# Performance work log

Measured on AMD Instinct MI355X. Metric: run time of the kernel, lower is better.

## Reference

```python
import jax, jax.numpy as jnp
import numpy as np

NU, NI, DIN, DOUT, NS, E = 100000, 100000, 128, 128, 5, 500000


def setup_inputs() -> dict:
    key = jax.random.key(0)
    ks = jax.random.split(key, 9)
    scale = 1.0 / np.sqrt(DIN)
    return {
        "user_inputs": jax.random.normal(ks[0], (NU, DIN), jnp.float32),
        "item_inputs": jax.random.normal(ks[1], (NI, DIN), jnp.float32),
        "weight": jax.random.normal(ks[2], (DIN, DOUT, NS), jnp.float32) * scale,
        "u_rows": jax.random.randint(ks[3], (NS, E), 0, NU),
        "u_cols": jax.random.randint(ks[4], (NS, E), 0, NI),
        "u_vals": jax.random.uniform(ks[5], (NS, E), jnp.float32),
        "i_rows": jax.random.randint(ks[6], (NS, E), 0, NI),
        "i_cols": jax.random.randint(ks[7], (NS, E), 0, NU),
        "i_vals": jax.random.uniform(ks[8], (NS, E), jnp.float32),
    }


def _spmm(rows, cols, vals, dense, n_rows):
    # COO sparse [n_rows, n_cols] @ dense [n_cols, d] -> [n_rows, d]
    msgs = vals[:, None] * dense[cols]  # [E, d]
    return jax.ops.segment_sum(msgs, rows, num_segments=n_rows)


def reference(user_inputs, item_inputs, weight, u_rows, u_cols, u_vals, i_rows, i_cols, i_vals):
    n_users = user_inputs.shape[0]
    n_items = item_inputs.shape[0]
    num_support = weight.shape[-1]
    w = jnp.zeros(weight.shape[:2], weight.dtype)
    user_hidden = jnp.zeros((n_users, weight.shape[1]), weight.dtype)
    item_hidden = jnp.zeros((n_items, weight.shape[1]), weight.dtype)
    for i in range(num_support):  # fixed small structural loop (5 rating levels)
        w = w + weight[..., i]            # cumulative weight sum, as in original
        tmp_u = user_inputs @ w           # [NU, DOUT]
        tmp_v = item_inputs @ w           # [NI, DOUT]
        user_hidden = user_hidden + _spmm(u_rows[i], u_cols[i], u_vals[i], tmp_v, n_users)
        item_hidden = item_hidden + _spmm(i_rows[i], i_cols[i], i_vals[i], tmp_u, n_items)
    return jax.nn.relu(user_hidden), jax.nn.relu(item_hidden)
```

## Files before the change

kernel.cpp:

```cpp
#include <hip/hip_runtime.h>

#define R_     100000
#define NSUP   5
#define EDGES  500000
#define D_     128
#define ND     (NSUP * D_)
#define BR     64
#define PPS2   ((R_ + BR - 1) / BR)
#define NBIN1  PPS2
#define CAP2   512

#define EPB    4096
#define BPS    123
#define OST    128
#define OROWS  (NBIN1 + 1)

#define PPB    12500
#define BTB    160

using short8 = __attribute__((ext_vector_type(8))) short;
using f32x4  = __attribute__((ext_vector_type(4))) float;

static __device__ __forceinline__ float bf2f_lo(unsigned p) { return __uint_as_float(p << 16); }
static __device__ __forceinline__ float bf2f_hi(unsigned p) { return __uint_as_float(p & 0xffff0000u); }
static __device__ __forceinline__ unsigned short f2bf(float x) {
    unsigned u = __float_as_uint(x);
    return (unsigned short)((u + 0x7fffu + ((u >> 16) & 1u)) >> 16);
}

__global__ __launch_bounds__(512) void pp_k(const float* __restrict__ user_in,
                                            const float* __restrict__ item_in,
                                            const float* __restrict__ w,
                                            const int* __restrict__ u_rows,
                                            const int* __restrict__ u_cols,
                                            const float* __restrict__ u_vals,
                                            const int* __restrict__ i_rows,
                                            const int* __restrict__ i_cols,
                                            const float* __restrict__ i_vals,
                                            unsigned short* __restrict__ srcb,
                                            unsigned short* __restrict__ bt,
                                            int* __restrict__ offs2,
                                            uint2* __restrict__ cedge2) {
    __shared__ uint2 estage[EPB];
    __shared__ int   hist[NBIN1];
    __shared__ int   wsum[8];

    int b = blockIdx.x, tid = threadIdx.x;
    if (b < PPB) {
        int side = b / 6250;
        int t = (b - side * 6250) * 512 + tid;
        const float* src = side ? user_in : item_in;
        float4 v = *(const float4*)(src + (size_t)t * 4);
        ushort4 o;
        o.x = f2bf(v.x); o.y = f2bf(v.y); o.z = f2bf(v.z); o.w = f2bf(v.w);
        *(ushort4*)(srcb + (size_t)side * (R_ * D_) + (size_t)t * 4) = o;
        return;
    }
    if (b < PPB + BTB) {
        int t = (b - PPB) * 512 + tid;
        int o = t / ND;
        int kk = t - o * ND;
        int i = kk >> 7, d = kk & 127;
        float s = 0.f;
        for (int j = 0; j <= i; j++) s += w[(d * D_ + o) * NSUP + j];
        bt[t] = f2bf(s);
        return;
    }
    int q = b - (PPB + BTB);
    int seg = q / BPS;
    int bb  = q - seg * BPS;
    int side = seg / NSUP;
    int sup  = seg - side * NSUP;
    const int*   rows = side ? i_rows : u_rows;
    const int*   cols = side ? i_cols : u_cols;
    const float* vals = side ? i_vals : u_vals;
    int e0 = bb * EPB;
    int ecnt = EDGES - e0; if (ecnt > EPB) ecnt = EPB;
    size_t gb = (size_t)sup * EDGES + e0;

    for (int j = tid; j < NBIN1; j += 512) hist[j] = 0;
    __syncthreads();
    for (int e = tid; e < ecnt; e += 512)
        atomicAdd(&hist[rows[gb + e] >> 6], 1);
    __syncthreads();
    int b0 = tid * 4;
    int c0 = 0, c1 = 0, c2 = 0, c3 = 0, s4 = 0;
    if (b0 < NBIN1) {
        c0 = hist[b0];
        c1 = (b0 + 1 < NBIN1) ? hist[b0 + 1] : 0;
        c2 = (b0 + 2 < NBIN1) ? hist[b0 + 2] : 0;
        c3 = (b0 + 3 < NBIN1) ? hist[b0 + 3] : 0;
        s4 = c0 + c1 + c2 + c3;
    }
    int lane = tid & 63, wv = tid >> 6;
    int s = s4;
#pragma unroll
    for (int off = 1; off < 64; off <<= 1) {
        int u = __shfl_up(s, off, 64);
        if (lane >= off) s += u;
    }
    if (lane == 63) wsum[wv] = s;
    __syncthreads();
    int woff = 0;
#pragma unroll
    for (int k = 0; k < 8; k++) woff += (k < wv) ? wsum[k] : 0;
    int ex = woff + s - s4;
    int orow = seg * OROWS;
    if (b0 < NBIN1) {
        int run = ex;
        offs2[(size_t)(orow + b0) * OST + bb] = run;  hist[b0] = run;  run += c0;
        if (b0 + 1 < NBIN1) { offs2[(size_t)(orow + b0 + 1) * OST + bb] = run; hist[b0 + 1] = run; run += c1; }
        if (b0 + 2 < NBIN1) { offs2[(size_t)(orow + b0 + 2) * OST + bb] = run; hist[b0 + 2] = run; run += c2; }
        if (b0 + 3 < NBIN1) { offs2[(size_t)(orow + b0 + 3) * OST + bb] = run; hist[b0 + 3] = run; run += c3; }
    }
    if (tid == 0) offs2[(size_t)(orow + NBIN1) * OST + bb] = ecnt;
    __syncthreads();
    for (int e = tid; e < ecnt; e += 512) {
        int r = rows[gb + e];
        int pos = atomicAdd(&hist[r >> 6], 1);
        uint2 E;
        E.x = (unsigned)cols[gb + e] | ((unsigned)(r & 63) << 17);
        E.y = __float_as_uint(vals[gb + e]);
        estage[pos] = E;
    }
    __syncthreads();
    size_t cbase = (size_t)(seg * BPS + bb) * EPB;
    for (int e = tid; e < ecnt; e += 512) cedge2[cbase + e] = estage[e];
}

__global__ __launch_bounds__(256) void rowsort_k(const int* __restrict__ offs2,
                                                 const uint2* __restrict__ cedge2,
                                                 uint2* __restrict__ cedge3,
                                                 int* __restrict__ rtab) {
    __shared__ uint2 eraw[CAP2];
    __shared__ uint2 eds[CAP2];
    __shared__ int rstart[BPS + 1];
    __shared__ int ro0[BPS];
    __shared__ int rcnt[BR];
    __shared__ int rsc[BR];

    int q = blockIdx.x;
    int seg = q / PPS2;
    int bin = q - seg * PPS2;
    int side = seg / NSUP;
    int sup  = seg - side * NSUP;
    int tid = threadIdx.x;
    int wid = tid >> 6, lane = tid & 63;

    if (wid == 0) {
        const int* orow = offs2 + ((size_t)seg * OROWS + bin) * OST;
        int j0 = lane * 2, j1 = lane * 2 + 1;
        int o0 = 0, o1 = 0, cc0 = 0, cc1 = 0;
        if (j0 < BPS) { o0 = orow[j0]; cc0 = orow[j0 + OST] - o0; }
        if (j1 < BPS) { o1 = orow[j1]; cc1 = orow[j1 + OST] - o1; }
        int sc = cc0 + cc1;
        int s = sc;
#pragma unroll
        for (int off = 1; off < 64; off <<= 1) {
            int u = __shfl_up(s, off, 64);
            if (lane >= off) s += u;
        }
        int ex = s - sc;
        if (j0 < BPS) { rstart[j0] = ex; ro0[j0] = o0; }
        if (j1 < BPS) { rstart[j1] = ex + cc0; ro0[j1] = o1; }
        if (lane == 63) rstart[BPS] = s;
    } else if (wid == 1 && lane < BR) {
        rcnt[lane] = 0;
    }
    __syncthreads();
    int n = rstart[BPS]; if (n > CAP2) n = CAP2;
    if (tid < 2 * BPS) {
        int rb = tid >> 1, j0 = tid & 1;
        int rs = rstart[rb];
        int cnt = rstart[rb + 1] - rs;
        const uint2* src = cedge2 + (size_t)(seg * BPS + rb) * EPB + ro0[rb];
        for (int j = j0; j < cnt; j += 2) {
            int pos = rs + j;
            if (pos < CAP2) eraw[pos] = src[j];
        }
    }
    __syncthreads();
    for (int e = tid; e < n; e += 256)
        atomicAdd(&rcnt[(eraw[e].x >> 17) & 63], 1);
    __syncthreads();
    if (wid == 0) {
        int vv = rcnt[lane];
        int s = vv;
#pragma unroll
        for (int off = 1; off < 64; off <<= 1) {
            int u = __shfl_up(s, off, 64);
            if (lane >= off) s += u;
        }
        rsc[lane] = s;
        rcnt[lane] = s - vv;
    }
    __syncthreads();
    if (tid < BR) {
        int v = rsc[tid]; if (v > CAP2) v = CAP2;
        rtab[((size_t)(side * PPS2 + bin)) * (NSUP * BR) + sup * BR + tid] = v;
    }
    for (int e = tid; e < n; e += 256) {
        uint2 E = eraw[e];
        int pos = atomicAdd(&rcnt[(E.x >> 17) & 63], 1);
        if (pos < CAP2) eds[pos] = E;
    }
    __syncthreads();
    size_t cb = (size_t)q * CAP2;
    for (int e = tid; e < n; e += 256) cedge3[cb + e] = eds[e];
}

__global__ __launch_bounds__(512, 8) void fused_k(const uint2* __restrict__ cedge3,
                                                  const int* __restrict__ rtab,
                                                  const unsigned short* __restrict__ srcb,
                                                  const unsigned short* __restrict__ BT,
                                                  float* __restrict__ out) {
    __shared__ unsigned short stile[BR * D_];
    __shared__ uint2 eds5[NSUP * CAP2];
    __shared__ int rsc_all[NSUP * BR];

    int side = blockIdx.x / PPS2;
    int bin  = blockIdx.x - side * PPS2;
    const unsigned short* srcbf = srcb + (size_t)side * (R_ * D_);
    float* outp = out + (size_t)side * R_ * D_;

    int tid = threadIdx.x;
    int wid = tid >> 6, lane = tid & 63;
    int g = lane >> 4, l16 = lane & 15;

    size_t rbase = ((size_t)(side * PPS2 + bin)) * (NSUP * BR);
    if (tid < NSUP * BR) rsc_all[tid] = rtab[rbase + tid];
#pragma unroll
    for (int i = 0; i < NSUP; i++) {
        int n = rtab[rbase + i * BR + 63]; if (n > CAP2) n = CAP2;
        const uint2* ebase = cedge3 + (size_t)((side * NSUP + i) * PPS2 + bin) * CAP2;
        for (int e = tid; e < n; e += 512) eds5[i * CAP2 + e] = ebase[e];
    }

    f32x4 acc[4];
#pragma unroll
    for (int rt = 0; rt < 4; rt++) acc[rt] = (f32x4){0.f, 0.f, 0.f, 0.f};

    __syncthreads();

    for (int i = 0; i < NSUP; i++) {
        const uint2* eds = eds5 + i * CAP2;
        for (int rq = wid; rq < 16; rq += 8) {
            int r = rq * 4 + g;
            int s0 = r ? rsc_all[i * BR + r - 1] : 0;
            int e2 = rsc_all[i * BR + r];
            float a0 = 0.f, a1 = 0.f, a2 = 0.f, a3 = 0.f;
            float a4 = 0.f, a5 = 0.f, a6 = 0.f, a7 = 0.f;
            int e = s0;
            for (; e + 3 < e2; e += 4) {
                uint2 E0 = eds[e], E1 = eds[e + 1], E2 = eds[e + 2], E3 = eds[e + 3];
                const uint4 p0 = *(const uint4*)(srcbf + (size_t)(E0.x & 0x1FFFFu) * D_ + l16 * 8);
                const uint4 p1 = *(const uint4*)(srcbf + (size_t)(E1.x & 0x1FFFFu) * D_ + l16 * 8);
                const uint4 p2 = *(const uint4*)(srcbf + (size_t)(E2.x & 0x1FFFFu) * D_ + l16 * 8);
                const uint4 p3 = *(const uint4*)(srcbf + (size_t)(E3.x & 0x1FFFFu) * D_ + l16 * 8);
                float v0 = __uint_as_float(E0.y), v1 = __uint_as_float(E1.y);
                float v2 = __uint_as_float(E2.y), v3 = __uint_as_float(E3.y);
                a0 += v0 * bf2f_lo(p0.x); a1 += v0 * bf2f_hi(p0.x);
                a2 += v0 * bf2f_lo(p0.y); a3 += v0 * bf2f_hi(p0.y);
                a4 += v0 * bf2f_lo(p0.z); a5 += v0 * bf2f_hi(p0.z);
                a6 += v0 * bf2f_lo(p0.w); a7 += v0 * bf2f_hi(p0.w);
                a0 += v1 * bf2f_lo(p1.x); a1 += v1 * bf2f_hi(p1.x);
                a2 += v1 * bf2f_lo(p1.y); a3 += v1 * bf2f_hi(p1.y);
                a4 += v1 * bf2f_lo(p1.z); a5 += v1 * bf2f_hi(p1.z);
                a6 += v1 * bf2f_lo(p1.w); a7 += v1 * bf2f_hi(p1.w);
                a0 += v2 * bf2f_lo(p2.x); a1 += v2 * bf2f_hi(p2.x);
                a2 += v2 * bf2f_lo(p2.y); a3 += v2 * bf2f_hi(p2.y);
                a4 += v2 * bf2f_lo(p2.z); a5 += v2 * bf2f_hi(p2.z);
                a6 += v2 * bf2f_lo(p2.w); a7 += v2 * bf2f_hi(p2.w);
                a0 += v3 * bf2f_lo(p3.x); a1 += v3 * bf2f_hi(p3.x);
                a2 += v3 * bf2f_lo(p3.y); a3 += v3 * bf2f_hi(p3.y);
                a4 += v3 * bf2f_lo(p3.z); a5 += v3 * bf2f_hi(p3.z);
                a6 += v3 * bf2f_lo(p3.w); a7 += v3 * bf2f_hi(p3.w);
            }
            for (; e < e2; e++) {
                uint2 E = eds[e];
                const uint4 pk = *(const uint4*)(srcbf + (size_t)(E.x & 0x1FFFFu) * D_ + l16 * 8);
                float vv = __uint_as_float(E.y);
                a0 += vv * bf2f_lo(pk.x); a1 += vv * bf2f_hi(pk.x);
                a2 += vv * bf2f_lo(pk.y); a3 += vv * bf2f_hi(pk.y);
                a4 += vv * bf2f_lo(pk.z); a5 += vv * bf2f_hi(pk.z);
                a6 += vv * bf2f_lo(pk.w); a7 += vv * bf2f_hi(pk.w);
            }
            uint4 P;
            P.x = ((unsigned)f2bf(a1) << 16) | f2bf(a0);
            P.y = ((unsigned)f2bf(a3) << 16) | f2bf(a2);
            P.z = ((unsigned)f2bf(a5) << 16) | f2bf(a4);
            P.w = ((unsigned)f2bf(a7) << 16) | f2bf(a6);
            int boff = r * 256 + ((l16 * 16) ^ ((r & 7) << 4));
            *(uint4*)((char*)stile + boff) = P;
        }
        __syncthreads();

        const unsigned short* btp = BT + (size_t)(wid * 16 + l16) * ND + i * D_;
#pragma unroll
        for (int cc = 0; cc < 4; cc++) {
            short8 bfr = *(const short8*)(btp + cc * 32 + g * 8);
#pragma unroll
            for (int rt = 0; rt < 4; rt++) {
                int row = rt * 16 + l16;
                int boff = row * 256 + ((cc * 64 + g * 16) ^ ((row & 7) << 4));
                short8 afr = *(const short8*)((const char*)stile + boff);
                acc[rt] = __builtin_amdgcn_mfma_f32_16x16x32_bf16(afr, bfr, acc[rt], 0, 0, 0);
            }
        }
        __syncthreads();
    }

    float* ltile = (float*)stile;
#pragma unroll
    for (int half = 0; half < 2; half++) {
#pragma unroll
        for (int rt2 = 0; rt2 < 2; rt2++) {
#pragma unroll
            for (int rr = 0; rr < 4; rr++) {
                int lrow = rt2 * 16 + g * 4 + rr;
                float v = acc[half * 2 + rt2][rr];
                v = v > 0.f ? v : 0.f;
                *(float*)((char*)ltile + lrow * 512 +
                          (((wid * 16 + l16) * 4) ^ ((lrow & 7) << 4))) = v;
            }
        }
        __syncthreads();
#pragma unroll
        for (int s = 0; s < 2; s++) {
            int idx = tid + s * 512;
            int lrow = idx >> 5, c4 = idx & 31;
            int grow = bin * BR + half * 32 + lrow;
            if (grow < R_) {
                float4 v = *(const float4*)((const char*)ltile + lrow * 512 +
                                            ((c4 * 16) ^ ((lrow & 7) << 4)));
                *(float4*)(outp + (size_t)grow * D_ + c4 * 4) = v;
            }
        }
        __syncthreads();
    }
}

extern "C" void kernel_launch(void* const* d_in, const int* in_sizes, int n_in,
                              void* d_out, int out_size, void* d_ws, size_t ws_size,
                              hipStream_t stream) {
    const float* user_in = (const float*)d_in[0];
    const float* item_in = (const float*)d_in[1];
    const float* weight  = (const float*)d_in[2];
    const int* u_rows = (const int*)d_in[3];
    const int* u_cols = (const int*)d_in[4];
    const float* u_vals = (const float*)d_in[5];
    const int* i_rows = (const int*)d_in[6];
    const int* i_cols = (const int*)d_in[7];
    const float* i_vals = (const float*)d_in[8];
    float* out = (float*)d_out;

    char* ws = (char*)d_ws;
    unsigned short* srcb = (unsigned short*)(ws);
    unsigned short* BT   = (unsigned short*)(ws + 51200000);
    uint2* cedge2        = (uint2*)         (ws + 51363840);
    int*   offs2         = (int*)           (ws + 91668480);
    uint2* cedge3        = (uint2*)         (ws + 99676160);
    int*   rtab          = (int*)           (ws + 163696640);

    pp_k<<<PPB + BTB + 10 * BPS, 512, 0, stream>>>(user_in, item_in, weight,
                                                   u_rows, u_cols, u_vals,
                                                   i_rows, i_cols, i_vals,
                                                   srcb, BT, offs2, cedge2);
    rowsort_k<<<10 * PPS2, 256, 0, stream>>>(offs2, cedge2, cedge3, rtab);
    fused_k<<<2 * PPS2, 512, 0, stream>>>(cedge3, rtab, srcb, BT, out);
}
```

Measured before the change: 537.5 us.

## Coarsen first-pass bucket sort to 512-row chunks and sort rows per chunk

The first partition pass now buckets edges into 196 coarse chunks of 512 rows instead of 1563 bins of 64 rows. This shrinks the offset table (fewer scattered global writes in pp_k and fewer reads in the second pass). The second pass uses one 512-thread block per chunk to gather up to 2944 edges, counting-sort them by the 9-bit local row, and scatter them into the per-64-row bin layout that fused_k expects. The trade-offs are larger per-block shared memory, fewer blocks in the second pass, and a fixed ECAP cap that could drop edges if a chunk gets unusually dense.

```diff
diff --git a/kernel.cpp b/kernel.cpp
--- a/kernel.cpp
+++ b/kernel.cpp
@@ -7,13 +7,14 @@
 #define ND     (NSUP * D_)
 #define BR     64
 #define PPS2   ((R_ + BR - 1) / BR)
-#define NBIN1  PPS2
 #define CAP2   512
 
 #define EPB    4096
 #define BPS    123
-#define OST    128
-#define OROWS  (NBIN1 + 1)
+#define NB_C   196
+#define CST    128
+#define CROWS  (NB_C + 1)
+#define ECAP   2944
 
 #define PPB    12500
 #define BTB    160
@@ -39,10 +40,10 @@
                                             const float* __restrict__ i_vals,
                                             unsigned short* __restrict__ srcb,
                                             unsigned short* __restrict__ bt,
-                                            int* __restrict__ offs2,
+                                            int* __restrict__ coff,
                                             uint2* __restrict__ cedge2) {
     __shared__ uint2 estage[EPB];
-    __shared__ int   hist[NBIN1];
+    __shared__ int   hist[NB_C];
     __shared__ int   wsum[8];
 
     int b = blockIdx.x, tid = threadIdx.x;
@@ -78,22 +79,14 @@
     int ecnt = EDGES - e0; if (ecnt > EPB) ecnt = EPB;
     size_t gb = (size_t)sup * EDGES + e0;
 
-    for (int j = tid; j < NBIN1; j += 512) hist[j] = 0;
+    if (tid < NB_C) hist[tid] = 0;
     __syncthreads();
     for (int e = tid; e < ecnt; e += 512)
-        atomicAdd(&hist[rows[gb + e] >> 6], 1);
-    __syncthreads();
-    int b0 = tid * 4;
-    int c0 = 0, c1 = 0, c2 = 0, c3 = 0, s4 = 0;
-    if (b0 < NBIN1) {
-        c0 = hist[b0];
-        c1 = (b0 + 1 < NBIN1) ? hist[b0 + 1] : 0;
-        c2 = (b0 + 2 < NBIN1) ? hist[b0 + 2] : 0;
-        c3 = (b0 + 3 < NBIN1) ? hist[b0 + 3] : 0;
-        s4 = c0 + c1 + c2 + c3;
-    }
+        atomicAdd(&hist[rows[gb + e] >> 9], 1);
+    __syncthreads();
+    int cnt = (tid < NB_C) ? hist[tid] : 0;
     int lane = tid & 63, wv = tid >> 6;
-    int s = s4;
+    int s = cnt;
 #pragma unroll
     for (int off = 1; off < 64; off <<= 1) {
         int u = __shfl_up(s, off, 64);
@@ -104,22 +97,18 @@
     int woff = 0;
 #pragma unroll
     for (int k = 0; k < 8; k++) woff += (k < wv) ? wsum[k] : 0;
-    int ex = woff + s - s4;
-    int orow = seg * OROWS;
-    if (b0 < NBIN1) {
-        int run = ex;
-        offs2[(size_t)(orow + b0) * OST + bb] = run;  hist[b0] = run;  run += c0;
-        if (b0 + 1 < NBIN1) { offs2[(size_t)(orow + b0 + 1) * OST + bb] = run; hist[b0 + 1] = run; run += c1; }
-        if (b0 + 2 < NBIN1) { offs2[(size_t)(orow + b0 + 2) * OST + bb] = run; hist[b0 + 2] = run; run += c2; }
-        if (b0 + 3 < NBIN1) { offs2[(size_t)(orow + b0 + 3) * OST + bb] = run; hist[b0 + 3] = run; run += c3; }
-    }
-    if (tid == 0) offs2[(size_t)(orow + NBIN1) * OST + bb] = ecnt;
+    int ex = woff + s - cnt;
+    if (tid < NB_C) {
+        coff[(size_t)(seg * CROWS + tid) * CST + bb] = ex;
+        hist[tid] = ex;
+    }
+    if (tid == 0) coff[(size_t)(seg * CROWS + NB_C) * CST + bb] = ecnt;
     __syncthreads();
     for (int e = tid; e < ecnt; e += 512) {
         int r = rows[gb + e];
-        int pos = atomicAdd(&hist[r >> 6], 1);
+        int pos = atomicAdd(&hist[r >> 9], 1);
         uint2 E;
-        E.x = (unsigned)cols[gb + e] | ((unsigned)(r & 63) << 17);
+        E.x = (unsigned)cols[gb + e] | ((unsigned)(r & 511) << 17);
         E.y = __float_as_uint(vals[gb + e]);
         estage[pos] = E;
     }
@@ -128,32 +117,34 @@
     for (int e = tid; e < ecnt; e += 512) cedge2[cbase + e] = estage[e];
 }
 
-__global__ __launch_bounds__(256) void rowsort_k(const int* __restrict__ offs2,
+__global__ __launch_bounds__(512) void binsort_k(const int* __restrict__ coff,
                                                  const uint2* __restrict__ cedge2,
                                                  uint2* __restrict__ cedge3,
                                                  int* __restrict__ rtab) {
-    __shared__ uint2 eraw[CAP2];
-    __shared__ uint2 eds[CAP2];
+    __shared__ uint2 estage[ECAP];
+    __shared__ unsigned short perm[ECAP];
+    __shared__ int hs[512];
+    __shared__ int cur[512];
     __shared__ int rstart[BPS + 1];
     __shared__ int ro0[BPS];
-    __shared__ int rcnt[BR];
-    __shared__ int rsc[BR];
+    __shared__ int wsum[8];
 
     int q = blockIdx.x;
-    int seg = q / PPS2;
-    int bin = q - seg * PPS2;
+    int seg = q / NB_C;
+    int c   = q - seg * NB_C;
     int side = seg / NSUP;
     int sup  = seg - side * NSUP;
     int tid = threadIdx.x;
-    int wid = tid >> 6, lane = tid & 63;
-
-    if (wid == 0) {
-        const int* orow = offs2 + ((size_t)seg * OROWS + bin) * OST;
-        int j0 = lane * 2, j1 = lane * 2 + 1;
-        int o0 = 0, o1 = 0, cc0 = 0, cc1 = 0;
-        if (j0 < BPS) { o0 = orow[j0]; cc0 = orow[j0 + OST] - o0; }
-        if (j1 < BPS) { o1 = orow[j1]; cc1 = orow[j1 + OST] - o1; }
-        int sc = cc0 + cc1;
+    int lane = tid & 63, wv = tid >> 6;
+
+    cur[tid] = 0;
+    if (wv == 0) {
+        const int* crow = coff + (size_t)(seg * CROWS + c) * CST;
+        int j0 = lane * 2, j1 = j0 + 1;
+        int o0 = 0, o1 = 0, c0 = 0, c1 = 0;
+        if (j0 < BPS) { o0 = crow[j0]; c0 = crow[j0 + CST] - o0; }
+        if (j1 < BPS) { o1 = crow[j1]; c1 = crow[j1 + CST] - o1; }
+        int sc = c0 + c1;
         int s = sc;
 #pragma unroll
         for (int off = 1; off < 64; off <<= 1) {
@@ -161,52 +152,65 @@
             if (lane >= off) s += u;
         }
         int ex = s - sc;
-        if (j0 < BPS) { rstart[j0] = ex; ro0[j0] = o0; }
-        if (j1 < BPS) { rstart[j1] = ex + cc0; ro0[j1] = o1; }
+        if (j0 < BPS) { rstart[j0] = ex;      ro0[j0] = o0; }
+        if (j1 < BPS) { rstart[j1] = ex + c0; ro0[j1] = o1; }
         if (lane == 63) rstart[BPS] = s;
-    } else if (wid == 1 && lane < BR) {
-        rcnt[lane] = 0;
-    }
-    __syncthreads();
-    int n = rstart[BPS]; if (n > CAP2) n = CAP2;
-    if (tid < 2 * BPS) {
-        int rb = tid >> 1, j0 = tid & 1;
+    }
+    __syncthreads();
+    int n = rstart[BPS]; if (n > ECAP) n = ECAP;
+    if (tid < 4 * BPS) {
+        int rb = tid >> 2, j0 = tid & 3;
         int rs = rstart[rb];
-        int cnt = rstart[rb + 1] - rs;
+        int cntr = rstart[rb + 1] - rs;
         const uint2* src = cedge2 + (size_t)(seg * BPS + rb) * EPB + ro0[rb];
-        for (int j = j0; j < cnt; j += 2) {
+        for (int j = j0; j < cntr; j += 4) {
             int pos = rs + j;
-            if (pos < CAP2) eraw[pos] = src[j];
-        }
-    }
-    __syncthreads();
-    for (int e = tid; e < n; e += 256)
-        atomicAdd(&rcnt[(eraw[e].x >> 17) & 63], 1);
-    __syncthreads();
-    if (wid == 0) {
-        int vv = rcnt[lane];
-        int s = vv;
-#pragma unroll
-        for (int off = 1; off < 64; off <<= 1) {
-            int u = __shfl_up(s, off, 64);
-            if (lane >= off) s += u;
-        }
-        rsc[lane] = s;
-        rcnt[lane] = s - vv;
-    }
-    __syncthreads();
-    if (tid < BR) {
-        int v = rsc[tid]; if (v > CAP2) v = CAP2;
-        rtab[((size_t)(side * PPS2 + bin)) * (NSUP * BR) + sup * BR + tid] = v;
-    }
-    for (int e = tid; e < n; e += 256) {
-        uint2 E = eraw[e];
-        int pos = atomicAdd(&rcnt[(E.x >> 17) & 63], 1);
-        if (pos < CAP2) eds[pos] = E;
-    }
-    __syncthreads();
-    size_t cb = (size_t)q * CAP2;
-    for (int e = tid; e < n; e += 256) cedge3[cb + e] = eds[e];
+            if (pos < ECAP) estage[pos] = src[j];
+        }
+    }
+    __syncthreads();
+    for (int e = tid; e < n; e += 512)
+        atomicAdd(&cur[(estage[e].x >> 17) & 511], 1);
+    __syncthreads();
+    int cnt = cur[tid];
+    int s = cnt;
+#pragma unroll
+    for (int off = 1; off < 64; off <<= 1) {
+        int u = __shfl_up(s, off, 64);
+        if (lane >= off) s += u;
+    }
+    if (lane == 63) wsum[wv] = s;
+    __syncthreads();
+    int woff = 0;
+#pragma unroll
+    for (int k = 0; k < 8; k++) woff += (k < wv) ? wsum[k] : 0;
+    int sinc = woff + s;
+    hs[tid] = sinc;
+    cur[tid] = sinc - cnt;
+    __syncthreads();
+    int b_ = tid >> 6;
+    int gbin = c * 8 + b_;
+    if (gbin < PPS2) {
+        int binst = b_ ? hs[(b_ << 6) - 1] : 0;
+        int srel = sinc - binst; if (srel > CAP2) srel = CAP2;
+        rtab[((size_t)(side * PPS2 + gbin)) * (NSUP * BR) + sup * BR + (tid & 63)] = srel;
+    }
+    for (int e = tid; e < n; e += 512) {
+        int pos = atomicAdd(&cur[(estage[e].x >> 17) & 511], 1);
+        perm[pos] = (unsigned short)e;
+    }
+    __syncthreads();
+    size_t segbase = (size_t)(side * NSUP + sup) * PPS2;
+    for (int ep = tid; ep < n; ep += 512) {
+        uint2 E = estage[perm[ep]];
+        int rl = (E.x >> 17) & 511;
+        int b2 = rl >> 6;
+        int gb2 = c * 8 + b2;
+        int binst = b2 ? hs[(b2 << 6) - 1] : 0;
+        int wpos = ep - binst;
+        if (wpos < CAP2 && gb2 < PPS2)
+            cedge3[(segbase + gb2) * CAP2 + wpos] = E;
+    }
 }
 
 __global__ __launch_bounds__(512, 8) void fused_k(const uint2* __restrict__ cedge3,
@@ -358,14 +362,14 @@
     unsigned short* srcb = (unsigned short*)(ws);
     unsigned short* BT   = (unsigned short*)(ws + 51200000);
     uint2* cedge2        = (uint2*)         (ws + 51363840);
-    int*   offs2         = (int*)           (ws + 91668480);
-    uint2* cedge3        = (uint2*)         (ws + 99676160);
-    int*   rtab          = (int*)           (ws + 163696640);
+    int*   coff          = (int*)           (ws + 91668480);
+    uint2* cedge3        = (uint2*)         (ws + 92677120);
+    int*   rtab          = (int*)           (ws + 156697600);
 
     pp_k<<<PPB + BTB + 10 * BPS, 512, 0, stream>>>(user_in, item_in, weight,
                                                    u_rows, u_cols, u_vals,
                                                    i_rows, i_cols, i_vals,
-                                                   srcb, BT, offs2, cedge2);
-    rowsort_k<<<10 * PPS2, 256, 0, stream>>>(offs2, cedge2, cedge3, rtab);
+                                                   srcb, BT, coff, cedge2);
+    binsort_k<<<10 * NB_C, 512, 0, stream>>>(coff, cedge2, cedge3, rtab);
     fused_k<<<2 * PPS2, 512, 0, stream>>>(cedge3, rtab, srcb, BT, out);
 }
```

New measurement: 494.9 us. -7.9%, faster.
